# Optimization experiments

Hardware: AMD Instinct MI355X
Metric: run time of the kernel (lower is better)

## Reference

```python
import jax, jax.numpy as jnp
import numpy as np

B, Q, C, NH, DH = 16, 300, 256, 8, 32
SPATIAL = [(80, 80), (40, 40), (20, 20), (10, 10)]
NPTS = [4, 4, 4, 4]
SUMP = sum(NPTS)
OFFSET_SCALE = 0.5


def _grid_bias():
    # directional init from build(): unit directions per head, scaled 1..n per level
    thetas = np.arange(NH) * (2.0 * np.pi / NH)
    g = np.stack([np.cos(thetas), np.sin(thetas)], -1)
    g = g / np.abs(g).max(-1, keepdims=True)
    g = np.tile(g[:, None, :], (1, SUMP, 1))
    scal = np.concatenate([np.arange(1, n + 1) for n in NPTS])[None, :, None]
    return (g * scal).astype(np.float32)


def setup_inputs() -> dict:
    key = jax.random.key(0)
    ks = jax.random.split(key, 5)
    S = sum(h * w for h, w in SPATIAL)
    return {
        "hidden_states": jax.random.normal(ks[0], (B, Q, C), jnp.float32),
        "encoder_hidden_states": jax.random.normal(ks[1], (B, S, C), jnp.float32),
        "reference_points": jax.random.uniform(ks[2], (B, Q, 1, 4), jnp.float32),
        "off_kernel": jax.random.normal(ks[3], (C, NH, SUMP, 2), jnp.float32) * 0.01,
        "off_bias": jnp.asarray(_grid_bias()),
        "attn_kernel": jax.random.normal(ks[4], (C, NH, SUMP), jnp.float32) * 0.01,
        "attn_bias": jnp.zeros((NH, SUMP), jnp.float32),
        "num_points_scale": jnp.asarray(
            np.concatenate([np.full(n, 1.0 / n) for n in NPTS]).astype(np.float32)
        ),
        "spatial_shapes": jnp.asarray(SPATIAL, jnp.int32),
    }


def _bilinear(v, loc, H, W):
    # v: [B, NH, H*W, DH]; loc: [B, Q, NH, P, 2] normalized in [0,1]
    # grid_sample(bilinear, align_corners=False, zeros padding) on grid 2*loc-1
    x = loc[..., 0] * W - 0.5
    y = loc[..., 1] * H - 0.5
    x0 = jnp.floor(x)
    y0 = jnp.floor(y)
    lx = x - x0
    ly = y - y0
    x0i = x0.astype(jnp.int32)
    y0i = y0.astype(jnp.int32)
    Bv = v.shape[0]
    Ql, Pl = loc.shape[1], loc.shape[3]
    out = jnp.zeros((Bv, NH, Ql, Pl, DH), v.dtype)
    corners = ((0, 0, (1 - lx) * (1 - ly)), (1, 0, lx * (1 - ly)),
               (0, 1, (1 - lx) * ly), (1, 1, lx * ly))
    for dx, dy, w in corners:
        xc = x0i + dx
        yc = y0i + dy
        valid = (xc >= 0) & (xc < W) & (yc >= 0) & (yc < H)
        idx = jnp.clip(yc, 0, H - 1) * W + jnp.clip(xc, 0, W - 1)  # [B,Q,NH,P]
        idx_t = jnp.transpose(idx, (0, 2, 1, 3)).reshape(Bv, NH, Ql * Pl, 1)
        g = jnp.take_along_axis(v, idx_t, axis=2).reshape(Bv, NH, Ql, Pl, DH)
        wt = (w * valid).astype(v.dtype)  # [B,Q,NH,P]
        out = out + g * jnp.transpose(wt, (0, 2, 1, 3))[..., None]
    return out  # [B,NH,Q,P,DH]


def reference(hidden_states, encoder_hidden_states, reference_points, off_kernel,
              off_bias, attn_kernel, attn_bias, num_points_scale, spatial_shapes):
    # sampling offsets / attention weights projections (EinsumDense equivalents)
    offsets = jnp.einsum('bqc,chpt->bqhpt', hidden_states, off_kernel) + off_bias
    attn = jax.nn.softmax(
        jnp.einsum('bqc,chp->bqhp', hidden_states, attn_kernel) + attn_bias, axis=-1)
    # 4-d reference points branch: center + scaled offsets * box wh
    center = jnp.expand_dims(reference_points[..., :2], -2)   # [B,Q,1,1,2]
    wh = jnp.expand_dims(reference_points[..., 2:], -2)       # [B,Q,1,1,2]
    loc = center + offsets * num_points_scale[:, None] * wh * OFFSET_SCALE  # [B,Q,NH,SUMP,2]
    S = encoder_hidden_states.shape[1]
    value = encoder_hidden_states.reshape(B, S, NH, DH).transpose(0, 2, 1, 3)  # [B,NH,S,DH]
    out = jnp.zeros((B, Q, NH, DH), hidden_states.dtype)
    start, pstart = 0, 0
    for (H, W), P in zip(SPATIAL, NPTS):
        v = value[:, :, start:start + H * W, :]
        l = loc[:, :, :, pstart:pstart + P, :]
        sampled = _bilinear(v, l, H, W)  # [B,NH,Q,P,DH]
        out = out + jnp.einsum('bhqpd,bqhp->bqhd', sampled,
                               attn[:, :, :, pstart:pstart + P])
        start += H * W
        pstart += P
    return out.reshape(B, Q, C), attn
```

## Files before the change

kernel.cpp:

```cpp
#include <hip/hip_runtime.h>
#include <math.h>

#define BB 16
#define QQ 300
#define CC 256
#define NHH 8
#define DHH 32
#define SUMPP 16
#define SSS 8500
#define GQ 10
#define QT (QQ / GQ)

__global__ __launch_bounds__(384) void precompute_kernel(
    const float* __restrict__ hs,
    const float* __restrict__ refp,
    const float* __restrict__ off_k,
    const float* __restrict__ off_b,
    const float* __restrict__ attn_k,
    const float* __restrict__ attn_b,
    const float* __restrict__ nps,
    float* __restrict__ loc_t,
    float* __restrict__ aw_t,
    float* __restrict__ attn_out)
{
    const int t = threadIdx.x;
    const int blk = blockIdx.x;
    const int b = blk / QT;
    const int q0 = (blk % QT) * GQ;
    const float* hsb = hs + ((size_t)b * QQ + q0) * CC;

    float acc[GQ];
#pragma unroll
    for (int g = 0; g < GQ; ++g) acc[g] = 0.f;

    if (t < 256) {
        const int h = t >> 5;
        const int p = (t >> 1) & 15;
        const int xy = t & 1;
        const float* kcol = off_k + t;
#pragma unroll 8
        for (int c = 0; c < CC; ++c) {
            const float k = kcol[c * 256];
#pragma unroll
            for (int g = 0; g < GQ; ++g)
                acc[g] = fmaf(hsb[g * CC + c], k, acc[g]);
        }
        const float scale = nps[p] * 0.5f;
        const float bias = off_b[t];
        const int didx = ((p * 8 + h) << 1) | xy;
#pragma unroll
        for (int g = 0; g < GQ; ++g) {
            const float4 r = *(const float4*)(refp + ((size_t)b * QQ + q0 + g) * 4);
            const float center = xy ? r.y : r.x;
            const float wh     = xy ? r.w : r.z;
            loc_t[((size_t)b * QQ + q0 + g) * 256 + didx] =
                fmaf((acc[g] + bias) * scale, wh, center);
        }
    } else {
        const int j = t - 256;
        const int h = j >> 4;
        const int p = j & 15;
        const float* kcol = attn_k + j;
#pragma unroll 8
        for (int c = 0; c < CC; ++c) {
            const float k = kcol[c * 128];
#pragma unroll
            for (int g = 0; g < GQ; ++g)
                acc[g] = fmaf(hsb[g * CC + c], k, acc[g]);
        }
        const float bias = attn_b[j];
#pragma unroll
        for (int g = 0; g < GQ; ++g) {
            const float logit = acc[g] + bias;
            float m = logit;
#pragma unroll
            for (int o = 1; o < 16; o <<= 1)
                m = fmaxf(m, __shfl_xor(m, o));
            const float e = __expf(logit - m);
            float s = e;
#pragma unroll
            for (int o = 1; o < 16; o <<= 1)
                s += __shfl_xor(s, o);
            const float a = e / s;
            attn_out[((size_t)b * QQ + q0 + g) * 128 + j] = a;
            aw_t[((size_t)b * QQ + q0 + g) * 128 + p * 8 + h] = a;
        }
    }
}

__global__ __launch_bounds__(256) void sample_kernel(
    const float* __restrict__ enc,
    const float2* __restrict__ loc2,
    const float* __restrict__ aw_t,
    float* __restrict__ out)
{
    __shared__ float4 sh_w[4 * 128];
    __shared__ int4   sh_o[4 * 128];

    const int g = blockIdx.x;
    const int xcd = g & 7;
    const int i = g >> 3;
    const int b = ((i & 1) << 3) | xcd;
    const int q0 = (i >> 1) * 4;
    const int qbase = b * QQ + q0;

    const int t = threadIdx.x;

#pragma unroll
    for (int k = 0; k < 2; ++k) {
        const int tau = t + k * 256;
        const int idx = tau & 127;
        const int p = idx >> 3;
        const int lvl = p >> 2;
        const int Wd = 80 >> lvl;
        const float Wf = (float)Wd;
        const int st = (25600 - (25600 >> (2 * lvl))) / 3;

        const float2 l = loc2[(size_t)qbase * 128 + tau];
        const float  a = aw_t[(size_t)qbase * 128 + tau];

        const float x = l.x * Wf - 0.5f;
        const float y = l.y * Wf - 0.5f;
        const float x0f = floorf(x), y0f = floorf(y);
        const float lx = x - x0f, ly = y - y0f;
        const int x0 = (int)x0f, y0 = (int)y0f;
        const int x1 = x0 + 1, y1 = y0 + 1;

        const bool vx0 = (unsigned)x0 < (unsigned)Wd;
        const bool vx1 = (unsigned)x1 < (unsigned)Wd;
        const bool vy0 = (unsigned)y0 < (unsigned)Wd;
        const bool vy1 = (unsigned)y1 < (unsigned)Wd;

        const int x0c = min(max(x0, 0), Wd - 1);
        const int x1c = min(max(x1, 0), Wd - 1);
        const int y0c = min(max(y0, 0), Wd - 1);
        const int y1c = min(max(y1, 0), Wd - 1);

        float w00 = (1.f - lx) * (1.f - ly) * a;
        float w10 = lx * (1.f - ly) * a;
        float w01 = (1.f - lx) * ly * a;
        float w11 = lx * ly * a;
        w00 = (vx0 & vy0) ? w00 : 0.f;
        w10 = (vx1 & vy0) ? w10 : 0.f;
        w01 = (vx0 & vy1) ? w01 : 0.f;
        w11 = (vx1 & vy1) ? w11 : 0.f;

        const int r0 = (st + y0c * Wd) << 10;
        const int r1 = (st + y1c * Wd) << 10;
        sh_w[tau] = make_float4(w00, w10, w01, w11);
        sh_o[tau] = make_int4(r0 + (x0c << 10), r0 + (x1c << 10),
                              r1 + (x0c << 10), r1 + (x1c << 10));
    }
    __syncthreads();

    const int qs = t >> 6;
    const int lane = t & 63;
    const int h = lane >> 3;
    const int d4 = (lane & 7) << 2;
    const char* vb = (const char*)(enc + b * (SSS * 256) + h * 32 + d4);

    float4 acc = {0.f, 0.f, 0.f, 0.f};

#pragma unroll
    for (int p = 0; p < 16; ++p) {
        const float4 w = sh_w[qs * 128 + p * 8 + h];
        const int4   o = sh_o[qs * 128 + p * 8 + h];
        const float4 v00 = *(const float4*)(vb + o.x);
        const float4 v10 = *(const float4*)(vb + o.y);
        const float4 v01 = *(const float4*)(vb + o.z);
        const float4 v11 = *(const float4*)(vb + o.w);
        acc.x = fmaf(w.x, v00.x, fmaf(w.y, v10.x, fmaf(w.z, v01.x, fmaf(w.w, v11.x, acc.x))));
        acc.y = fmaf(w.x, v00.y, fmaf(w.y, v10.y, fmaf(w.z, v01.y, fmaf(w.w, v11.y, acc.y))));
        acc.z = fmaf(w.x, v00.z, fmaf(w.y, v10.z, fmaf(w.z, v01.z, fmaf(w.w, v11.z, acc.z))));
        acc.w = fmaf(w.x, v00.w, fmaf(w.y, v10.w, fmaf(w.z, v01.w, fmaf(w.w, v11.w, acc.w))));
    }

    float* op = out + (size_t)(qbase + qs) * 256 + h * 32 + d4;
    *(float4*)op = acc;
}

extern "C" void kernel_launch(void* const* d_in, const int* in_sizes, int n_in,
                              void* d_out, int out_size, void* d_ws, size_t ws_size,
                              hipStream_t stream) {
    const float* hs     = (const float*)d_in[0];
    const float* enc    = (const float*)d_in[1];
    const float* refp   = (const float*)d_in[2];
    const float* off_k  = (const float*)d_in[3];
    const float* off_b  = (const float*)d_in[4];
    const float* attn_k = (const float*)d_in[5];
    const float* attn_b = (const float*)d_in[6];
    const float* nps    = (const float*)d_in[7];

    float* out      = (float*)d_out;
    float* attn_out = out + (size_t)BB * QQ * CC;
    float* loc_t    = (float*)d_ws;
    float* aw_t     = loc_t + (size_t)BB * QQ * 256;

    precompute_kernel<<<BB * QT, 384, 0, stream>>>(hs, refp, off_k, off_b,
                                                   attn_k, attn_b, nps,
                                                   loc_t, aw_t, attn_out);
    sample_kernel<<<BB * (QQ / 4), 256, 0, stream>>>(enc, (const float2*)loc_t,
                                                     aw_t, out);
}
```

Before: 244.2 us.

## Fuse projection/softmax precompute with bilinear sampling into one kernel

Merges the offset/attention projection kernel and the sampling kernel into a single 640-thread kernel. Each block handles 10 queries and keeps locations and attention weights in shared memory instead of a global workspace. This removes one launch and a global write/read round trip. In exchange, each block's sampling must wait for its projection phase, 256 threads sit idle during the projection phase, and there are fewer, larger blocks. The block-to-batch mapping also changes so blocks of the same batch share an XCD.

```diff
diff --git a/kernel.cpp b/kernel.cpp
--- a/kernel.cpp
+++ b/kernel.cpp
@@ -5,122 +5,109 @@
 #define QQ 300
 #define CC 256
 #define NHH 8
-#define DHH 32
-#define SUMPP 16
 #define SSS 8500
 #define GQ 10
 #define QT (QQ / GQ)
 
-__global__ __launch_bounds__(384) void precompute_kernel(
+__global__ __launch_bounds__(640) void fused_kernel(
     const float* __restrict__ hs,
+    const float* __restrict__ enc,
     const float* __restrict__ refp,
     const float* __restrict__ off_k,
     const float* __restrict__ off_b,
     const float* __restrict__ attn_k,
     const float* __restrict__ attn_b,
     const float* __restrict__ nps,
-    float* __restrict__ loc_t,
-    float* __restrict__ aw_t,
+    float* __restrict__ out,
     float* __restrict__ attn_out)
 {
+    __shared__ float  sh_l[GQ * 128 * 2];
+    __shared__ float  sh_a[GQ * 128];
+    __shared__ float4 sh_w[GQ * 128];
+    __shared__ int4   sh_o[GQ * 128];
+
     const int t = threadIdx.x;
     const int blk = blockIdx.x;
-    const int b = blk / QT;
-    const int q0 = (blk % QT) * GQ;
+    const int b = blk & 15;
+    const int q0 = (blk >> 4) * GQ;
     const float* hsb = hs + ((size_t)b * QQ + q0) * CC;
 
-    float acc[GQ];
+    if (t < 384) {
+        float acc[GQ];
 #pragma unroll
-    for (int g = 0; g < GQ; ++g) acc[g] = 0.f;
+        for (int g = 0; g < GQ; ++g) acc[g] = 0.f;
 
-    if (t < 256) {
-        const int h = t >> 5;
-        const int p = (t >> 1) & 15;
-        const int xy = t & 1;
-        const float* kcol = off_k + t;
+        if (t < 256) {
+            const int h = t >> 5;
+            const int p = (t >> 1) & 15;
+            const int xy = t & 1;
+            const float* kcol = off_k + t;
 #pragma unroll 8
-        for (int c = 0; c < CC; ++c) {
-            const float k = kcol[c * 256];
+            for (int c = 0; c < CC; ++c) {
+                const float k = kcol[c * 256];
 #pragma unroll
-            for (int g = 0; g < GQ; ++g)
-                acc[g] = fmaf(hsb[g * CC + c], k, acc[g]);
-        }
-        const float scale = nps[p] * 0.5f;
-        const float bias = off_b[t];
-        const int didx = ((p * 8 + h) << 1) | xy;
+                for (int g = 0; g < GQ; ++g)
+                    acc[g] = fmaf(hsb[g * CC + c], k, acc[g]);
+            }
+            const float scale = nps[p] * 0.5f;
+            const float bias = off_b[t];
+            const int didx = ((p * 8 + h) << 1) | xy;
 #pragma unroll
-        for (int g = 0; g < GQ; ++g) {
-            const float4 r = *(const float4*)(refp + ((size_t)b * QQ + q0 + g) * 4);
-            const float center = xy ? r.y : r.x;
-            const float wh     = xy ? r.w : r.z;
-            loc_t[((size_t)b * QQ + q0 + g) * 256 + didx] =
-                fmaf((acc[g] + bias) * scale, wh, center);
-        }
-    } else {
-        const int j = t - 256;
-        const int h = j >> 4;
-        const int p = j & 15;
-        const float* kcol = attn_k + j;
+            for (int g = 0; g < GQ; ++g) {
+                const float4 r = *(const float4*)(refp + ((size_t)b * QQ + q0 + g) * 4);
+                const float center = xy ? r.y : r.x;
+                const float wh     = xy ? r.w : r.z;
+                sh_l[g * 256 + didx] = fmaf((acc[g] + bias) * scale, wh, center);
+            }
+        } else {
+            const int j = t - 256;
+            const int h = j >> 4;
+            const int p = j & 15;
+            const float* kcol = attn_k + j;
 #pragma unroll 8
-        for (int c = 0; c < CC; ++c) {
-            const float k = kcol[c * 128];
+            for (int c = 0; c < CC; ++c) {
+                const float k = kcol[c * 128];
 #pragma unroll
-            for (int g = 0; g < GQ; ++g)
-                acc[g] = fmaf(hsb[g * CC + c], k, acc[g]);
-        }
-        const float bias = attn_b[j];
+                for (int g = 0; g < GQ; ++g)
+                    acc[g] = fmaf(hsb[g * CC + c], k, acc[g]);
+            }
+            const float bias = attn_b[j];
 #pragma unroll
-        for (int g = 0; g < GQ; ++g) {
-            const float logit = acc[g] + bias;
-            float m = logit;
+            for (int g = 0; g < GQ; ++g) {
+                const float logit = acc[g] + bias;
+                float m = logit;
 #pragma unroll
-            for (int o = 1; o < 16; o <<= 1)
-                m = fmaxf(m, __shfl_xor(m, o));
-            const float e = __expf(logit - m);
-            float s = e;
+                for (int o = 1; o < 16; o <<= 1)
+                    m = fmaxf(m, __shfl_xor(m, o));
+                const float e = __expf(logit - m);
+                float s = e;
 #pragma unroll
-            for (int o = 1; o < 16; o <<= 1)
-                s += __shfl_xor(s, o);
-            const float a = e / s;
-            attn_out[((size_t)b * QQ + q0 + g) * 128 + j] = a;
-            aw_t[((size_t)b * QQ + q0 + g) * 128 + p * 8 + h] = a;
+                for (int o = 1; o < 16; o <<= 1)
+                    s += __shfl_xor(s, o);
+                const float a = e / s;
+                attn_out[((size_t)b * QQ + q0 + g) * 128 + j] = a;
+                sh_a[g * 128 + p * 8 + h] = a;
+            }
         }
     }
-}
-
-__global__ __launch_bounds__(256) void sample_kernel(
-    const float* __restrict__ enc,
-    const float2* __restrict__ loc2,
-    const float* __restrict__ aw_t,
-    float* __restrict__ out)
-{
-    __shared__ float4 sh_w[4 * 128];
-    __shared__ int4   sh_o[4 * 128];
-
-    const int g = blockIdx.x;
-    const int xcd = g & 7;
-    const int i = g >> 3;
-    const int b = ((i & 1) << 3) | xcd;
-    const int q0 = (i >> 1) * 4;
-    const int qbase = b * QQ + q0;
-
-    const int t = threadIdx.x;
+    __syncthreads();
 
 #pragma unroll
     for (int k = 0; k < 2; ++k) {
-        const int tau = t + k * 256;
+        const int tau = t + k * 640;
         const int idx = tau & 127;
         const int p = idx >> 3;
         const int lvl = p >> 2;
         const int Wd = 80 >> lvl;
         const float Wf = (float)Wd;
-        const int st = (25600 - (25600 >> (2 * lvl))) / 3;
+        const int st = (lvl == 0) ? 0 : (lvl == 1) ? 6400 : (lvl == 2) ? 8000 : 8400;
 
-        const float2 l = loc2[(size_t)qbase * 128 + tau];
-        const float  a = aw_t[(size_t)qbase * 128 + tau];
+        const float lx_ = sh_l[tau * 2];
+        const float ly_ = sh_l[tau * 2 + 1];
+        const float a = sh_a[tau];
 
-        const float x = l.x * Wf - 0.5f;
-        const float y = l.y * Wf - 0.5f;
+        const float x = lx_ * Wf - 0.5f;
+        const float y = ly_ * Wf - 0.5f;
         const float x0f = floorf(x), y0f = floorf(y);
         const float lx = x - x0f, ly = y - y0f;
         const int x0 = (int)x0f, y0 = (int)y0f;
@@ -159,7 +146,7 @@
     const int d4 = (lane & 7) << 2;
     const char* vb = (const char*)(enc + b * (SSS * 256) + h * 32 + d4);
 
-    float4 acc = {0.f, 0.f, 0.f, 0.f};
+    float4 acc4 = {0.f, 0.f, 0.f, 0.f};
 
 #pragma unroll
     for (int p = 0; p < 16; ++p) {
@@ -169,14 +156,14 @@
         const float4 v10 = *(const float4*)(vb + o.y);
         const float4 v01 = *(const float4*)(vb + o.z);
         const float4 v11 = *(const float4*)(vb + o.w);
-        acc.x = fmaf(w.x, v00.x, fmaf(w.y, v10.x, fmaf(w.z, v01.x, fmaf(w.w, v11.x, acc.x))));
-        acc.y = fmaf(w.x, v00.y, fmaf(w.y, v10.y, fmaf(w.z, v01.y, fmaf(w.w, v11.y, acc.y))));
-        acc.z = fmaf(w.x, v00.z, fmaf(w.y, v10.z, fmaf(w.z, v01.z, fmaf(w.w, v11.z, acc.z))));
-        acc.w = fmaf(w.x, v00.w, fmaf(w.y, v10.w, fmaf(w.z, v01.w, fmaf(w.w, v11.w, acc.w))));
+        acc4.x = fmaf(w.x, v00.x, fmaf(w.y, v10.x, fmaf(w.z, v01.x, fmaf(w.w, v11.x, acc4.x))));
+        acc4.y = fmaf(w.x, v00.y, fmaf(w.y, v10.y, fmaf(w.z, v01.y, fmaf(w.w, v11.y, acc4.y))));
+        acc4.z = fmaf(w.x, v00.z, fmaf(w.y, v10.z, fmaf(w.z, v01.z, fmaf(w.w, v11.z, acc4.z))));
+        acc4.w = fmaf(w.x, v00.w, fmaf(w.y, v10.w, fmaf(w.z, v01.w, fmaf(w.w, v11.w, acc4.w))));
     }
 
-    float* op = out + (size_t)(qbase + qs) * 256 + h * 32 + d4;
-    *(float4*)op = acc;
+    float* op = out + ((size_t)b * QQ + q0 + qs) * 256 + h * 32 + d4;
+    *(float4*)op = acc4;
 }
 
 extern "C" void kernel_launch(void* const* d_in, const int* in_sizes, int n_in,
@@ -193,12 +180,8 @@
 
     float* out      = (float*)d_out;
     float* attn_out = out + (size_t)BB * QQ * CC;
-    float* loc_t    = (float*)d_ws;
-    float* aw_t     = loc_t + (size_t)BB * QQ * 256;
 
-    precompute_kernel<<<BB * QT, 384, 0, stream>>>(hs, refp, off_k, off_b,
-                                                   attn_k, attn_b, nps,
-                                                   loc_t, aw_t, attn_out);
-    sample_kernel<<<BB * (QQ / 4), 256, 0, stream>>>(enc, (const float2*)loc_t,
-                                                     aw_t, out);
+    fused_kernel<<<BB * QT, 640, 0, stream>>>(hs, enc, refp, off_k, off_b,
+                                              attn_k, attn_b, nps,
+                                              out, attn_out);
 }
```

Result: slower. 256.4 us (+5.0%).

## Convert encoder values to fp16 in prep kernel and gather half-precision values

Applied to the files above, without the earlier changes.

Adds a grid-stride conversion pass to the precompute launch that writes the whole encoder tensor as fp16 into workspace. The sampling kernel then gathers 8-byte half4 values instead of 16-byte float4 values and widens them to fp32 before accumulating. The aim is to halve the bytes per bilinear gather. The cost is a full read of the fp32 encoder tensor plus a write of the fp16 copy on every call, and reduced value precision. It also shrinks the per-block query group of the precompute stage and hardcodes the level start offsets.

```diff
diff --git a/kernel.cpp b/kernel.cpp
--- a/kernel.cpp
+++ b/kernel.cpp
@@ -1,30 +1,57 @@
 #include <hip/hip_runtime.h>
+#include <hip/hip_fp16.h>
 #include <math.h>
 
 #define BB 16
 #define QQ 300
 #define CC 256
 #define NHH 8
-#define DHH 32
-#define SUMPP 16
 #define SSS 8500
-#define GQ 10
+#define GQ 6
 #define QT (QQ / GQ)
-
-__global__ __launch_bounds__(384) void precompute_kernel(
+#define PRE_BLOCKS (BB * QT)
+#define CONV_U4 4352000
+#define CONV_BLOCKS 2834
+#define CONV_THREADS (CONV_BLOCKS * 384)
+
+__global__ __launch_bounds__(384) void prep_kernel(
     const float* __restrict__ hs,
+    const float* __restrict__ enc,
     const float* __restrict__ refp,
     const float* __restrict__ off_k,
     const float* __restrict__ off_b,
     const float* __restrict__ attn_k,
     const float* __restrict__ attn_b,
     const float* __restrict__ nps,
+    __half* __restrict__ enc16,
     float* __restrict__ loc_t,
     float* __restrict__ aw_t,
     float* __restrict__ attn_out)
 {
     const int t = threadIdx.x;
     const int blk = blockIdx.x;
+
+    if (blk >= PRE_BLOCKS) {
+        const int cb = blk - PRE_BLOCKS;
+        const float4* src = (const float4*)enc;
+        uint4* dst = (uint4*)enc16;
+        for (int i = cb * 384 + t; i < CONV_U4; i += CONV_THREADS) {
+            const float4 a0 = src[2 * i];
+            const float4 a1 = src[2 * i + 1];
+            const __half2 h0 = __floats2half2_rn(a0.x, a0.y);
+            const __half2 h1 = __floats2half2_rn(a0.z, a0.w);
+            const __half2 h2 = __floats2half2_rn(a1.x, a1.y);
+            const __half2 h3 = __floats2half2_rn(a1.z, a1.w);
+            uint4 o;
+            o.x = *(const unsigned*)&h0;
+            o.y = *(const unsigned*)&h1;
+            o.z = *(const unsigned*)&h2;
+            o.w = *(const unsigned*)&h3;
+            dst[i] = o;
+        }
+        return;
+    }
+
     const int b = blk / QT;
     const int q0 = (blk % QT) * GQ;
     const float* hsb = hs + ((size_t)b * QQ + q0) * CC;
@@ -56,7 +83,7 @@
             loc_t[((size_t)b * QQ + q0 + g) * 256 + didx] =
                 fmaf((acc[g] + bias) * scale, wh, center);
         }
-    } else {
+    } else if (t < 384) {
         const int j = t - 256;
         const int h = j >> 4;
         const int p = j & 15;
@@ -89,7 +116,7 @@
 }
 
 __global__ __launch_bounds__(256) void sample_kernel(
-    const float* __restrict__ enc,
+    const __half* __restrict__ enc16,
     const float2* __restrict__ loc2,
     const float* __restrict__ aw_t,
     float* __restrict__ out)
@@ -114,7 +141,7 @@
         const int lvl = p >> 2;
         const int Wd = 80 >> lvl;
         const float Wf = (float)Wd;
-        const int st = (25600 - (25600 >> (2 * lvl))) / 3;
+        const int st = (lvl == 0) ? 0 : (lvl == 1) ? 6400 : (lvl == 2) ? 8000 : 8400;
 
         const float2 l = loc2[(size_t)qbase * 128 + tau];
         const float  a = aw_t[(size_t)qbase * 128 + tau];
@@ -145,19 +172,19 @@
         w01 = (vx0 & vy1) ? w01 : 0.f;
         w11 = (vx1 & vy1) ? w11 : 0.f;
 
-        const int r0 = (st + y0c * Wd) << 10;
-        const int r1 = (st + y1c * Wd) << 10;
+        const int r0 = (st + y0c * Wd) << 9;
+        const int r1 = (st + y1c * Wd) << 9;
         sh_w[tau] = make_float4(w00, w10, w01, w11);
-        sh_o[tau] = make_int4(r0 + (x0c << 10), r0 + (x1c << 10),
-                              r1 + (x0c << 10), r1 + (x1c << 10));
+        sh_o[tau] = make_int4(r0 + (x0c << 9), r0 + (x1c << 9),
+                              r1 + (x0c << 9), r1 + (x1c << 9));
     }
     __syncthreads();
 
     const int qs = t >> 6;
     const int lane = t & 63;
     const int h = lane >> 3;
-    const int d4 = (lane & 7) << 2;
-    const char* vb = (const char*)(enc + b * (SSS * 256) + h * 32 + d4);
+    const int d4 = lane & 7;
+    const char* vb = (const char*)enc16 + (size_t)b * (SSS * 512) + (h << 6) + (d4 << 3);
 
     float4 acc = {0.f, 0.f, 0.f, 0.f};
 
@@ -165,17 +192,27 @@
     for (int p = 0; p < 16; ++p) {
         const float4 w = sh_w[qs * 128 + p * 8 + h];
         const int4   o = sh_o[qs * 128 + p * 8 + h];
-        const float4 v00 = *(const float4*)(vb + o.x);
-        const float4 v10 = *(const float4*)(vb + o.y);
-        const float4 v01 = *(const float4*)(vb + o.z);
-        const float4 v11 = *(const float4*)(vb + o.w);
-        acc.x = fmaf(w.x, v00.x, fmaf(w.y, v10.x, fmaf(w.z, v01.x, fmaf(w.w, v11.x, acc.x))));
-        acc.y = fmaf(w.x, v00.y, fmaf(w.y, v10.y, fmaf(w.z, v01.y, fmaf(w.w, v11.y, acc.y))));
-        acc.z = fmaf(w.x, v00.z, fmaf(w.y, v10.z, fmaf(w.z, v01.z, fmaf(w.w, v11.z, acc.z))));
-        acc.w = fmaf(w.x, v00.w, fmaf(w.y, v10.w, fmaf(w.z, v01.w, fmaf(w.w, v11.w, acc.w))));
-    }
-
-    float* op = out + (size_t)(qbase + qs) * 256 + h * 32 + d4;
+        const uint2 u00 = *(const uint2*)(vb + o.x);
+        const uint2 u10 = *(const uint2*)(vb + o.y);
+        const uint2 u01 = *(const uint2*)(vb + o.z);
+        const uint2 u11 = *(const uint2*)(vb + o.w);
+
+        const float2 a00 = __half22float2(*(const __half2*)&u00.x);
+        const float2 b00 = __half22float2(*(const __half2*)&u00.y);
+        const float2 a10 = __half22float2(*(const __half2*)&u10.x);
+        const float2 b10 = __half22float2(*(const __half2*)&u10.y);
+        const float2 a01 = __half22float2(*(const __half2*)&u01.x);
+        const float2 b01 = __half22float2(*(const __half2*)&u01.y);
+        const float2 a11 = __half22float2(*(const __half2*)&u11.x);
+        const float2 b11 = __half22float2(*(const __half2*)&u11.y);
+
+        acc.x = fmaf(w.x, a00.x, fmaf(w.y, a10.x, fmaf(w.z, a01.x, fmaf(w.w, a11.x, acc.x))));
+        acc.y = fmaf(w.x, a00.y, fmaf(w.y, a10.y, fmaf(w.z, a01.y, fmaf(w.w, a11.y, acc.y))));
+        acc.z = fmaf(w.x, b00.x, fmaf(w.y, b10.x, fmaf(w.z, b01.x, fmaf(w.w, b11.x, acc.z))));
+        acc.w = fmaf(w.x, b00.y, fmaf(w.y, b10.y, fmaf(w.z, b01.y, fmaf(w.w, b11.y, acc.w))));
+    }
+
+    float* op = out + (size_t)(qbase + qs) * 256 + (h << 5) + (d4 << 2);
     *(float4*)op = acc;
 }
 
@@ -193,12 +230,14 @@
 
     float* out      = (float*)d_out;
     float* attn_out = out + (size_t)BB * QQ * CC;
-    float* loc_t    = (float*)d_ws;
-    float* aw_t     = loc_t + (size_t)BB * QQ * 256;
-
-    precompute_kernel<<<BB * QT, 384, 0, stream>>>(hs, refp, off_k, off_b,
-                                                   attn_k, attn_b, nps,
-                                                   loc_t, aw_t, attn_out);
-    sample_kernel<<<BB * (QQ / 4), 256, 0, stream>>>(enc, (const float2*)loc_t,
-                                                     aw_t, out);
+
+    __half* enc16 = (__half*)d_ws;
+    float* loc_t  = (float*)((char*)d_ws + 69632000);
+    float* aw_t   = loc_t + (size_t)BB * QQ * 256;
+
+    prep_kernel<<<PRE_BLOCKS + CONV_BLOCKS, 384, 0, stream>>>(
+        hs, enc, refp, off_k, off_b, attn_k, attn_b, nps,
+        enc16, loc_t, aw_t, attn_out);
+    sample_kernel<<<BB * (QQ / 4), 256, 0, stream>>>(
+        enc16, (const float2*)loc_t, aw_t, out);
 }
```

Measured after the change: 257.7 us. 1.05x slower.

## Move bilinear weight/offset computation into precompute; shrink sample blocks to one query

Applied to the files above, without the earlier changes.

The bilinear corner weights and byte offsets are now computed in the precompute kernel from shared-memory locations and attention weights, and written to global float4/int4 arrays. The sampling kernel becomes a 64-thread, one-query-per-block gather that reads these precomputed values directly. This removes the per-block setup phase and barrier in the sampling kernel and gives it finer-grained blocks. In exchange, the intermediate written to the workspace is larger (32 bytes per sample instead of 12) and far more tiny blocks are launched.

```diff
diff --git a/kernel.cpp b/kernel.cpp
--- a/kernel.cpp
+++ b/kernel.cpp
@@ -5,8 +5,6 @@
 #define QQ 300
 #define CC 256
 #define NHH 8
-#define DHH 32
-#define SUMPP 16
 #define SSS 8500
 #define GQ 10
 #define QT (QQ / GQ)
@@ -19,10 +17,13 @@
     const float* __restrict__ attn_k,
     const float* __restrict__ attn_b,
     const float* __restrict__ nps,
-    float* __restrict__ loc_t,
-    float* __restrict__ aw_t,
+    float4* __restrict__ w_arr,
+    int4*  __restrict__ o_arr,
     float* __restrict__ attn_out)
 {
+    __shared__ float sh_l[GQ * 128 * 2];
+    __shared__ float sh_a[GQ * 128];
+
     const int t = threadIdx.x;
     const int blk = blockIdx.x;
     const int b = blk / QT;
@@ -53,8 +54,7 @@
             const float4 r = *(const float4*)(refp + ((size_t)b * QQ + q0 + g) * 4);
             const float center = xy ? r.y : r.x;
             const float wh     = xy ? r.w : r.z;
-            loc_t[((size_t)b * QQ + q0 + g) * 256 + didx] =
-                fmaf((acc[g] + bias) * scale, wh, center);
+            sh_l[g * 256 + didx] = fmaf((acc[g] + bias) * scale, wh, center);
         }
     } else {
         const int j = t - 256;
@@ -83,44 +83,26 @@
                 s += __shfl_xor(s, o);
             const float a = e / s;
             attn_out[((size_t)b * QQ + q0 + g) * 128 + j] = a;
-            aw_t[((size_t)b * QQ + q0 + g) * 128 + p * 8 + h] = a;
+            sh_a[g * 128 + p * 8 + h] = a;
         }
     }
-}
-
-__global__ __launch_bounds__(256) void sample_kernel(
-    const float* __restrict__ enc,
-    const float2* __restrict__ loc2,
-    const float* __restrict__ aw_t,
-    float* __restrict__ out)
-{
-    __shared__ float4 sh_w[4 * 128];
-    __shared__ int4   sh_o[4 * 128];
-
-    const int g = blockIdx.x;
-    const int xcd = g & 7;
-    const int i = g >> 3;
-    const int b = ((i & 1) << 3) | xcd;
-    const int q0 = (i >> 1) * 4;
-    const int qbase = b * QQ + q0;
-
-    const int t = threadIdx.x;
-
-#pragma unroll
-    for (int k = 0; k < 2; ++k) {
-        const int tau = t + k * 256;
+    __syncthreads();
+
+    const size_t gbase = ((size_t)b * QQ + q0) * 128;
+    for (int tau = t; tau < GQ * 128; tau += 384) {
         const int idx = tau & 127;
         const int p = idx >> 3;
         const int lvl = p >> 2;
         const int Wd = 80 >> lvl;
         const float Wf = (float)Wd;
-        const int st = (25600 - (25600 >> (2 * lvl))) / 3;
-
-        const float2 l = loc2[(size_t)qbase * 128 + tau];
-        const float  a = aw_t[(size_t)qbase * 128 + tau];
-
-        const float x = l.x * Wf - 0.5f;
-        const float y = l.y * Wf - 0.5f;
+        const int st = (lvl == 0) ? 0 : (lvl == 1) ? 6400 : (lvl == 2) ? 8000 : 8400;
+
+        const float lxs = sh_l[tau * 2];
+        const float lys = sh_l[tau * 2 + 1];
+        const float a = sh_a[tau];
+
+        const float x = lxs * Wf - 0.5f;
+        const float y = lys * Wf - 0.5f;
         const float x0f = floorf(x), y0f = floorf(y);
         const float lx = x - x0f, ly = y - y0f;
         const int x0 = (int)x0f, y0 = (int)y0f;
@@ -147,24 +129,39 @@
 
         const int r0 = (st + y0c * Wd) << 10;
         const int r1 = (st + y1c * Wd) << 10;
-        sh_w[tau] = make_float4(w00, w10, w01, w11);
-        sh_o[tau] = make_int4(r0 + (x0c << 10), r0 + (x1c << 10),
-                              r1 + (x0c << 10), r1 + (x1c << 10));
+        w_arr[gbase + tau] = make_float4(w00, w10, w01, w11);
+        o_arr[gbase + tau] = make_int4(r0 + (x0c << 10), r0 + (x1c << 10),
+                                       r1 + (x0c << 10), r1 + (x1c << 10));
     }
-    __syncthreads();
-
-    const int qs = t >> 6;
-    const int lane = t & 63;
+}
+
+__global__ __launch_bounds__(64) void sample_kernel(
+    const float* __restrict__ enc,
+    const float4* __restrict__ w_arr,
+    const int4*  __restrict__ o_arr,
+    float* __restrict__ out)
+{
+    const int g = blockIdx.x;
+    const int xcd = g & 7;
+    const int i = g >> 3;
+    const int b = ((i & 1) << 3) | xcd;
+    const int q = i >> 1;
+    const size_t mbase = ((size_t)b * QQ + q) * 128;
+
+    const int lane = threadIdx.x;
     const int h = lane >> 3;
     const int d4 = (lane & 7) << 2;
-    const char* vb = (const char*)(enc + b * (SSS * 256) + h * 32 + d4);
+    const char* vb = (const char*)(enc + (size_t)b * (SSS * 256) + h * 32 + d4);
+
+    const float4* wp = w_arr + mbase + h;
+    const int4*  op = o_arr + mbase + h;
 
     float4 acc = {0.f, 0.f, 0.f, 0.f};
 
 #pragma unroll
     for (int p = 0; p < 16; ++p) {
-        const float4 w = sh_w[qs * 128 + p * 8 + h];
-        const int4   o = sh_o[qs * 128 + p * 8 + h];
+        const float4 w = wp[p * 8];
+        const int4   o = op[p * 8];
         const float4 v00 = *(const float4*)(vb + o.x);
         const float4 v10 = *(const float4*)(vb + o.y);
         const float4 v01 = *(const float4*)(vb + o.z);
@@ -175,8 +172,8 @@
         acc.w = fmaf(w.x, v00.w, fmaf(w.y, v10.w, fmaf(w.z, v01.w, fmaf(w.w, v11.w, acc.w))));
     }
 
-    float* op = out + (size_t)(qbase + qs) * 256 + h * 32 + d4;
-    *(float4*)op = acc;
+    float* outp = out + ((size_t)b * QQ + q) * 256 + h * 32 + d4;
+    *(float4*)outp = acc;
 }
 
 extern "C" void kernel_launch(void* const* d_in, const int* in_sizes, int n_in,
@@ -193,12 +190,12 @@
 
     float* out      = (float*)d_out;
     float* attn_out = out + (size_t)BB * QQ * CC;
-    float* loc_t    = (float*)d_ws;
-    float* aw_t     = loc_t + (size_t)BB * QQ * 256;
+
+    float4* w_arr = (float4*)d_ws;
+    int4*   o_arr = (int4*)((char*)d_ws + (size_t)BB * QQ * 128 * 16);
 
     precompute_kernel<<<BB * QT, 384, 0, stream>>>(hs, refp, off_k, off_b,
                                                    attn_k, attn_b, nps,
-                                                   loc_t, aw_t, attn_out);
-    sample_kernel<<<BB * (QQ / 4), 256, 0, stream>>>(enc, (const float2*)loc_t,
-                                                     aw_t, out);
+                                                   w_arr, o_arr, attn_out);
+    sample_kernel<<<BB * QQ, 64, 0, stream>>>(enc, w_arr, o_arr, out);
 }
```

Result: no change. 246.6 us (+1.0%).
